# Optimization experiments

Hardware: AMD Instinct MI355X
Metric: run time of the kernel (lower is better)

## Reference

```python
import jax, jax.numpy as jnp
import numpy as np

NUM_HEADS = 16  # init kwarg num_attention_heads


def setup_inputs() -> dict:
    key = jax.random.key(0)
    k1, k2, k3, k4 = jax.random.split(key, 4)
    B, T, E = 2, 2048, 1024
    query = jax.random.normal(k1, (B, T, E), dtype=jnp.float32)
    key_t = jax.random.normal(k2, (B, T, E), dtype=jnp.float32)
    value = jax.random.normal(k3, (B, T, E), dtype=jnp.float32)
    # final output projection (nn.Linear(hidden, hidden, bias=False)); torch stores [out,in]
    W_out = jax.random.normal(k4, (E, E), dtype=jnp.float32) * 0.02
    return {"query": query, "key": key_t, "value": value, "W_out": W_out}


def reference(query, key, value, W_out):
    # NOTE: in the source, the per-head q_i/k_i/v_i linear projections are
    # overwritten by reshapes of the raw inputs, so the qs/ks/vs weights are
    # dead code. Every head computes identical output; mean over heads is a
    # no-op. We reproduce that exact math here.
    B, T, E = query.shape
    H = NUM_HEADS
    d = E // H  # head_dim; also d_k used in the 1/sqrt(d_k) scaling

    def split_heads(x):  # [B,T,E] -> [B,H,T,d]
        return x.reshape(B, T, H, d).transpose(0, 2, 1, 3)

    q = split_heads(query)
    k = split_heads(key)
    v = split_heads(value)

    scale = jnp.sqrt(jnp.asarray(d, dtype=jnp.float32))
    scores = jnp.einsum('bhtd,bhsd->bhts', q, k) / scale  # [B,H,T,T]
    attn = jax.nn.softmax(scores, axis=-1)
    head = jnp.einsum('bhts,bhsd->bhtd', attn, v)         # [B,H,T,d]
    head = head.transpose(0, 2, 1, 3).reshape(B, T, E)    # concat heads

    # mean over H identical head outputs == head; final linear (no bias)
    outputs = head @ W_out.T                              # [B,T,E]
    # mean over H identical attention maps == attn, returned as [B*H,T,T]
    attention = attn.reshape(B * H, T, T)
    return outputs, attention
```

## Files before the change

kernel.cpp:

```cpp
#include <hip/hip_runtime.h>
#include <hip/hip_fp16.h>

#define B_NUM  2
#define T_DIM  2048
#define E_DIM  1024
#define H_NUM  16
#define D_HEAD 64
#define BH_NUM (B_NUM * H_NUM)
#define NT     (T_DIM / 64)

using half8  = __attribute__((ext_vector_type(8))) _Float16;
using half4v = __attribute__((ext_vector_type(4))) _Float16;
using f32x4  = __attribute__((ext_vector_type(4))) float;

#define AS1 __attribute__((address_space(1)))
#define AS3 __attribute__((address_space(3)))

#define QSCALE 0.18033688011112042f

#define BAR_VM(N)                                                       \
    do {                                                                \
        asm volatile("s_waitcnt vmcnt(" #N ")" ::: "memory");           \
        __builtin_amdgcn_s_barrier();                                   \
        __builtin_amdgcn_sched_barrier(0);                              \
    } while (0)

__device__ __forceinline__ void bar_plain() {
    __builtin_amdgcn_s_barrier();
    __builtin_amdgcn_sched_barrier(0);
}

#define TP_BLOCKS  (NT * BH_NUM)
#define CAST_BLOCKS 1280
__global__ void prep_kernel(const float* __restrict__ kin,
                            const float* __restrict__ win,
                            const float* __restrict__ V,
                            _Float16* __restrict__ Kh,
                            _Float16* __restrict__ Wh,
                            _Float16* __restrict__ Vt,
                            int nk4, int ntot4) {
    __shared__ float tile[64][65];
    int t = threadIdx.x;

    if (blockIdx.x < TP_BLOCKS) {
        int s0 = (blockIdx.x & 31) * 64;
        int bh = blockIdx.x >> 5;
        int b = bh >> 4, h = bh & 15;

        int row = t >> 2;
        int c0  = (t & 3) * 16;
        const float* src = V + ((size_t)(b * T_DIM + s0 + row)) * E_DIM + h * D_HEAD + c0;
#pragma unroll
        for (int j = 0; j < 16; j += 4) {
            float4 v = *reinterpret_cast<const float4*>(src + j);
            tile[row][c0 + j + 0] = v.x;
            tile[row][c0 + j + 1] = v.y;
            tile[row][c0 + j + 2] = v.z;
            tile[row][c0 + j + 3] = v.w;
        }
        __syncthreads();

        int d  = t >> 2;
        int sc = (t & 3) * 16;
        half8 h0, h1;
#pragma unroll
        for (int j = 0; j < 8; ++j) {
            h0[j] = (_Float16)tile[sc + j][d];
            h1[j] = (_Float16)tile[sc + 8 + j][d];
        }
        _Float16* dst = Vt + ((size_t)(bh * D_HEAD + d)) * T_DIM + s0 + sc;
        *reinterpret_cast<half8*>(dst)     = h0;
        *reinterpret_cast<half8*>(dst + 8) = h1;
    } else {
        int stride = CAST_BLOCKS * 256;
        for (int i = (blockIdx.x - TP_BLOCKS) * 256 + t; i < ntot4; i += stride) {
            const float* src = (i < nk4) ? kin : win;
            _Float16* dst    = (i < nk4) ? Kh  : Wh;
            int j            = (i < nk4) ? i   : i - nk4;
            float4 v = reinterpret_cast<const float4*>(src)[j];
            half4v hh;
            hh[0] = (_Float16)v.x; hh[1] = (_Float16)v.y;
            hh[2] = (_Float16)v.z; hh[3] = (_Float16)v.w;
            reinterpret_cast<half4v*>(dst)[j] = hh;
        }
    }
}

__device__ __forceinline__ void stage_gl(const _Float16* __restrict__ g,
                                         size_t stride, _Float16* lds,
                                         int w, int lane) {
    int r0 = lane >> 3;
    int c  = (lane & 7) ^ r0;
#pragma unroll
    for (int j = 0; j < 2; ++j) {
        int r = (w + 4 * j) * 8 + r0;
        const _Float16* src = g + (size_t)r * stride + c * 8;
        _Float16* dst = lds + (w + 4 * j) * 512;
        __builtin_amdgcn_global_load_lds((const AS1 void*)src, (AS3 void*)dst,
                                         16, 0, 0);
    }
}

__device__ __forceinline__ half8 read_frag64(const _Float16* lds, int row, int chunk) {
    int csw = chunk ^ (row & 7);
    return *reinterpret_cast<const half8*>(lds + row * 64 + csw * 8);
}

__device__ __forceinline__ void load_qfrag(const float* qsrc, int lg, half8* qf) {
#pragma unroll
    for (int ks = 0; ks < 2; ++ks) {
        float4 a0 = *reinterpret_cast<const float4*>(qsrc + (lg + 4 * ks) * 8);
        float4 a1 = *reinterpret_cast<const float4*>(qsrc + (lg + 4 * ks) * 8 + 4);
        qf[ks][0] = (_Float16)(a0.x * QSCALE); qf[ks][1] = (_Float16)(a0.y * QSCALE);
        qf[ks][2] = (_Float16)(a0.z * QSCALE); qf[ks][3] = (_Float16)(a0.w * QSCALE);
        qf[ks][4] = (_Float16)(a1.x * QSCALE); qf[ks][5] = (_Float16)(a1.y * QSCALE);
        qf[ks][6] = (_Float16)(a1.z * QSCALE); qf[ks][7] = (_Float16)(a1.w * QSCALE);
    }
}

__global__ __launch_bounds__(256) void attn_kernel(
        const float* __restrict__ Q, const _Float16* __restrict__ Kh,
        const _Float16* __restrict__ Vt, float* __restrict__ attn_out,
        _Float16* __restrict__ head_h) {
    __shared__ __align__(16) _Float16 kbuf[2][64 * 64];
    __shared__ __align__(16) _Float16 vbuf[2][64 * 64];
    __shared__ __align__(16) _Float16 pbuf[4][16 * 64];

    int tid  = threadIdx.x;
    int wq   = tid >> 6;
    int lane = tid & 63;
    int l15  = lane & 15;
    int lg   = lane >> 4;

    int flat = blockIdx.x;
    int bh   = (flat & 7) * 4 + (flat >> 8);
    int qt   = (flat >> 3) & 31;
    int q0   = qt * 64;
    int b = bh >> 4, h = bh & 15;

    const float* qsrc = Q + ((size_t)(b * T_DIM + q0 + wq * 16 + l15)) * E_DIM + h * D_HEAD;
    half8 qfrag[2];
    load_qfrag(qsrc, lg, qfrag);

    const _Float16* kg = Kh + ((size_t)b * T_DIM) * E_DIM + h * D_HEAD;
    const _Float16* vg = Vt + (size_t)bh * D_HEAD * T_DIM;

#define P1TILE(KB)                                                             \
    {                                                                          \
        f32x4 acc[4];                                                          \
        _Pragma("unroll")                                                      \
        for (int ct = 0; ct < 4; ++ct) acc[ct] = (f32x4){0.f, 0.f, 0.f, 0.f};  \
        __builtin_amdgcn_s_setprio(1);                                         \
        _Pragma("unroll")                                                      \
        for (int ks = 0; ks < 2; ++ks)                                         \
            _Pragma("unroll")                                                  \
            for (int ct = 0; ct < 4; ++ct) {                                   \
                half8 kf = read_frag64((KB), ct * 16 + l15, lg + 4 * ks);      \
                acc[ct] = __builtin_amdgcn_mfma_f32_16x16x32_f16(              \
                    kf, qfrag[ks], acc[ct], 0, 0, 0);                          \
            }                                                                  \
        __builtin_amdgcn_s_setprio(0);                                         \
        _Pragma("unroll")                                                      \
        for (int ct = 0; ct < 4; ++ct)                                         \
            _Pragma("unroll")                                                  \
            for (int r = 0; r < 4; ++r)                                        \
                lsum += __builtin_amdgcn_exp2f(acc[ct][r]);                    \
    }

    int rot2 = (qt << 1) & 31;
#define IDX1(n) (((n) + rot2) & 31)
    float lsum = 0.0f;
    stage_gl(kg + (size_t)IDX1(0) * 64 * E_DIM, E_DIM, kbuf[0], wq, lane);
    stage_gl(kg + (size_t)IDX1(1) * 64 * E_DIM, E_DIM, kbuf[1], wq, lane);
    for (int tt = 0; tt < NT / 2; tt += 2) {
        {
            stage_gl(kg + (size_t)IDX1(2 * tt + 2) * 64 * E_DIM, E_DIM, vbuf[0], wq, lane);
            stage_gl(kg + (size_t)IDX1(2 * tt + 3) * 64 * E_DIM, E_DIM, vbuf[1], wq, lane);
            BAR_VM(4);
            P1TILE(kbuf[0]);
            P1TILE(kbuf[1]);
            bar_plain();
        }
        {
            if (tt + 2 < NT / 2) {
                stage_gl(kg + (size_t)IDX1(2 * tt + 4) * 64 * E_DIM, E_DIM, kbuf[0], wq, lane);
                stage_gl(kg + (size_t)IDX1(2 * tt + 5) * 64 * E_DIM, E_DIM, kbuf[1], wq, lane);
                BAR_VM(4);
            } else {
                BAR_VM(0);
            }
            P1TILE(vbuf[0]);
            P1TILE(vbuf[1]);
            bar_plain();
        }
    }
#undef IDX1

    lsum += __shfl_xor(lsum, 16);
    lsum += __shfl_xor(lsum, 32);
    float rl = 1.0f / lsum;

    f32x4 oacc[4];
#pragma unroll
    for (int cd = 0; cd < 4; ++cd) oacc[cd] = (f32x4){0.f, 0.f, 0.f, 0.f};

    float* ab = attn_out + (size_t)bh * T_DIM * T_DIM;
    _Float16* pw = pbuf[wq];
    int myq = q0 + wq * 16 + l15;

    int cur = 0;
    {
        int p0 = qt & 31;
        stage_gl(kg + (size_t)p0 * 64 * E_DIM, E_DIM, kbuf[0], wq, lane);
        stage_gl(vg + p0 * 64, T_DIM, vbuf[0], wq, lane);
    }
    for (int t = 0; t < NT; ++t) {
        int phys = (t + qt) & 31;
        if (t < NT - 1) {
            int pn = (t + 1 + qt) & 31;
            stage_gl(kg + (size_t)pn * 64 * E_DIM, E_DIM, kbuf[cur ^ 1], wq, lane);
            stage_gl(vg + pn * 64, T_DIM, vbuf[cur ^ 1], wq, lane);
        }
        if (t == 0)           BAR_VM(4);
        else if (t < NT - 1)  BAR_VM(8);
        else                  BAR_VM(4);
        const _Float16* kb = kbuf[cur];
        const _Float16* vb = vbuf[cur];

        f32x4 acc[4];
#pragma unroll
        for (int ct = 0; ct < 4; ++ct) acc[ct] = (f32x4){0.f, 0.f, 0.f, 0.f};
        __builtin_amdgcn_s_setprio(1);
#pragma unroll
        for (int ks = 0; ks < 2; ++ks)
#pragma unroll
            for (int ct = 0; ct < 4; ++ct) {
                half8 kf = read_frag64(kb, ct * 16 + l15, lg + 4 * ks);
                acc[ct] = __builtin_amdgcn_mfma_f32_16x16x32_f16(kf, qfrag[ks], acc[ct], 0, 0, 0);
            }
        __builtin_amdgcn_s_setprio(0);

        float* abrow = ab + (size_t)myq * T_DIM + phys * 64 + lg * 4;
#pragma unroll
        for (int ct = 0; ct < 4; ++ct) {
            f32x4 p;
            p[0] = __builtin_amdgcn_exp2f(acc[ct][0]) * rl;
            p[1] = __builtin_amdgcn_exp2f(acc[ct][1]) * rl;
            p[2] = __builtin_amdgcn_exp2f(acc[ct][2]) * rl;
            p[3] = __builtin_amdgcn_exp2f(acc[ct][3]) * rl;
            *reinterpret_cast<f32x4*>(abrow + ct * 16) = p;
            half4v ph;
            ph[0] = (_Float16)p[0]; ph[1] = (_Float16)p[1];
            ph[2] = (_Float16)p[2]; ph[3] = (_Float16)p[3];
            int cc = (ct * 4 + lg) ^ l15;
            *reinterpret_cast<half4v*>(pw + l15 * 64 + cc * 4) = ph;
        }

        __builtin_amdgcn_s_setprio(1);
#pragma unroll
        for (int ks = 0; ks < 2; ++ks) {
            int c0 = 2 * (lg + 4 * ks);
            half4v lo = *reinterpret_cast<const half4v*>(pw + l15 * 64 + ((c0)     ^ l15) * 4);
            half4v hi = *reinterpret_cast<const half4v*>(pw + l15 * 64 + ((c0 + 1) ^ l15) * 4);
            half8 pa;
            pa[0] = lo[0]; pa[1] = lo[1]; pa[2] = lo[2]; pa[3] = lo[3];
            pa[4] = hi[0]; pa[5] = hi[1]; pa[6] = hi[2]; pa[7] = hi[3];
#pragma unroll
            for (int cd = 0; cd < 4; ++cd) {
                half8 vf = read_frag64(vb, cd * 16 + l15, lg + 4 * ks);
                oacc[cd] = __builtin_amdgcn_mfma_f32_16x16x32_f16(pa, vf, oacc[cd], 0, 0, 0);
            }
        }
        __builtin_amdgcn_s_setprio(0);
        bar_plain();
        cur ^= 1;
    }

    _Float16* hw = head_h + ((size_t)(b * T_DIM + q0 + wq * 16)) * E_DIM + h * D_HEAD;
#pragma unroll
    for (int cd = 0; cd < 4; ++cd)
#pragma unroll
        for (int r = 0; r < 4; ++r) {
            int qm = lg * 4 + r;
            hw[(size_t)qm * E_DIM + cd * 16 + l15] = (_Float16)oacc[cd][r];
        }
#undef P1TILE
}

__global__ __launch_bounds__(256) void proj_kernel(
        const _Float16* __restrict__ A, const _Float16* __restrict__ Wh,
        float* __restrict__ out) {
    __shared__ __align__(16) _Float16 abuf[2][64 * 64];
    __shared__ __align__(16) _Float16 bbuf[2][64 * 64];

    int tid  = threadIdx.x;
    int wq   = tid >> 6;
    int lane = tid & 63;
    int l15  = lane & 15;
    int lg   = lane >> 4;

    int m0 = blockIdx.x * 64;
    int n0 = blockIdx.y * 64;

    f32x4 acc[4];
#pragma unroll
    for (int ct = 0; ct < 4; ++ct) acc[ct] = (f32x4){0.f, 0.f, 0.f, 0.f};

    int cur = 0;
    stage_gl(A  + (size_t)m0 * E_DIM, E_DIM, abuf[0], wq, lane);
    stage_gl(Wh + (size_t)n0 * E_DIM, E_DIM, bbuf[0], wq, lane);
    for (int t = 0; t < E_DIM / 64; ++t) {
        if (t + 1 < E_DIM / 64) {
            stage_gl(A  + (size_t)m0 * E_DIM + (t + 1) * 64, E_DIM, abuf[cur ^ 1], wq, lane);
            stage_gl(Wh + (size_t)n0 * E_DIM + (t + 1) * 64, E_DIM, bbuf[cur ^ 1], wq, lane);
            BAR_VM(4);
        } else {
            BAR_VM(0);
        }
#pragma unroll
        for (int ks = 0; ks < 2; ++ks) {
            half8 hf = read_frag64(abuf[cur], wq * 16 + l15, lg + 4 * ks);
#pragma unroll
            for (int ct = 0; ct < 4; ++ct) {
                half8 wf = read_frag64(bbuf[cur], ct * 16 + l15, lg + 4 * ks);
                acc[ct] = __builtin_amdgcn_mfma_f32_16x16x32_f16(wf, hf, acc[ct], 0, 0, 0);
            }
        }
        bar_plain();
        cur ^= 1;
    }

    float* orow = out + (size_t)(m0 + wq * 16 + l15) * E_DIM + n0 + lg * 4;
#pragma unroll
    for (int ct = 0; ct < 4; ++ct) {
        f32x4 o;
        o[0] = acc[ct][0]; o[1] = acc[ct][1]; o[2] = acc[ct][2]; o[3] = acc[ct][3];
        *reinterpret_cast<f32x4*>(orow + ct * 16) = o;
    }
}

extern "C" void kernel_launch(void* const* d_in, const int* in_sizes, int n_in,
                              void* d_out, int out_size, void* d_ws, size_t ws_size,
                              hipStream_t stream) {
    const float* q = (const float*)d_in[0];
    const float* k = (const float*)d_in[1];
    const float* v = (const float*)d_in[2];
    const float* w = (const float*)d_in[3];

    float* outs = (float*)d_out;
    float* attn = outs + (size_t)B_NUM * T_DIM * E_DIM;

    char* ws = (char*)d_ws;
    _Float16* Kh = (_Float16*)(ws);
    _Float16* Vt = (_Float16*)(ws + (size_t)(8  << 20));
    _Float16* Wh = (_Float16*)(ws + (size_t)(16 << 20));
    _Float16* Hh = (_Float16*)(ws + (size_t)(18 << 20));

    int nk4 = B_NUM * T_DIM * E_DIM / 4;
    int nw4 = E_DIM * E_DIM / 4;

    prep_kernel<<<TP_BLOCKS + CAST_BLOCKS, 256, 0, stream>>>(
        k, w, v, Kh, Wh, Vt, nk4, nk4 + nw4);
    attn_kernel<<<NT * BH_NUM, 256, 0, stream>>>(q, Kh, Vt, attn, Hh);
    proj_kernel<<<dim3((B_NUM * T_DIM) / 64, E_DIM / 64), 256, 0, stream>>>(Hh, Wh, outs);
}
```

Before: 183.5 us.

## Use five-slot ring buffer for softmax-denominator pass, reuse smem across phases

Replaces the separate K/V/P shared buffers with one 5-slot shared pool. The first pass, which computes row sums, now streams K tiles through a 5-deep ring with a prefetch distance of three and one barrier per tile, replacing the double-buffered pairs with two barriers per pair. The second pass reuses the same slots for K, V and P. The goal is to hide more global load latency in pass one and keep shared memory usage the same or lower. The trade-off is a selection chain to pick the ring slot and an extra barrier between the phases.

```diff
diff --git a/kernel.cpp b/kernel.cpp
--- a/kernel.cpp
+++ b/kernel.cpp
@@ -122,9 +122,8 @@
         const float* __restrict__ Q, const _Float16* __restrict__ Kh,
         const _Float16* __restrict__ Vt, float* __restrict__ attn_out,
         _Float16* __restrict__ head_h) {
-    __shared__ __align__(16) _Float16 kbuf[2][64 * 64];
-    __shared__ __align__(16) _Float16 vbuf[2][64 * 64];
-    __shared__ __align__(16) _Float16 pbuf[4][16 * 64];
+    __shared__ __align__(16) _Float16 smem[5 * 4096];
+#define SLOTP(s) (smem + (s) * 4096)
 
     int tid  = threadIdx.x;
     int wq   = tid >> 6;
@@ -167,34 +166,35 @@
                 lsum += __builtin_amdgcn_exp2f(acc[ct][r]);                    \
     }
 
-    int rot2 = (qt << 1) & 31;
-#define IDX1(n) (((n) + rot2) & 31)
+#define SLOTSEL(s) ((s) == 0 ? SLOTP(0) : (s) == 1 ? SLOTP(1) :                \
+                    (s) == 2 ? SLOTP(2) : (s) == 3 ? SLOTP(3) : SLOTP(4))
+
     float lsum = 0.0f;
-    stage_gl(kg + (size_t)IDX1(0) * 64 * E_DIM, E_DIM, kbuf[0], wq, lane);
-    stage_gl(kg + (size_t)IDX1(1) * 64 * E_DIM, E_DIM, kbuf[1], wq, lane);
-    for (int tt = 0; tt < NT / 2; tt += 2) {
-        {
-            stage_gl(kg + (size_t)IDX1(2 * tt + 2) * 64 * E_DIM, E_DIM, vbuf[0], wq, lane);
-            stage_gl(kg + (size_t)IDX1(2 * tt + 3) * 64 * E_DIM, E_DIM, vbuf[1], wq, lane);
-            BAR_VM(4);
-            P1TILE(kbuf[0]);
-            P1TILE(kbuf[1]);
-            bar_plain();
-        }
-        {
-            if (tt + 2 < NT / 2) {
-                stage_gl(kg + (size_t)IDX1(2 * tt + 4) * 64 * E_DIM, E_DIM, kbuf[0], wq, lane);
-                stage_gl(kg + (size_t)IDX1(2 * tt + 5) * 64 * E_DIM, E_DIM, kbuf[1], wq, lane);
-                BAR_VM(4);
-            } else {
-                BAR_VM(0);
-            }
-            P1TILE(vbuf[0]);
-            P1TILE(vbuf[1]);
-            bar_plain();
-        }
-    }
+    {
+#define IDX1(n) (((n) + qt) & 31)
+        stage_gl(kg + (size_t)IDX1(0) * 64 * E_DIM, E_DIM, SLOTP(0), wq, lane);
+        stage_gl(kg + (size_t)IDX1(1) * 64 * E_DIM, E_DIM, SLOTP(1), wq, lane);
+        stage_gl(kg + (size_t)IDX1(2) * 64 * E_DIM, E_DIM, SLOTP(2), wq, lane);
+        int ss = 3, sc = 0;
+        for (int t = 0; t <= NT - 4; ++t) {
+            _Float16* sp = SLOTSEL(ss);
+            stage_gl(kg + (size_t)IDX1(t + 3) * 64 * E_DIM, E_DIM, sp, wq, lane);
+            BAR_VM(6);
+            const _Float16* cp = SLOTSEL(sc);
+            P1TILE(cp);
+            ss = (ss == 4) ? 0 : ss + 1;
+            sc = (sc == 4) ? 0 : sc + 1;
+        }
+        BAR_VM(4);
+        { const _Float16* cp = SLOTSEL(sc); P1TILE(cp); }
+        sc = (sc == 4) ? 0 : sc + 1;
+        BAR_VM(2);
+        { const _Float16* cp = SLOTSEL(sc); P1TILE(cp); }
+        sc = (sc == 4) ? 0 : sc + 1;
+        BAR_VM(0);
+        { const _Float16* cp = SLOTSEL(sc); P1TILE(cp); }
 #undef IDX1
+    }
 
     lsum += __shfl_xor(lsum, 16);
     lsum += __shfl_xor(lsum, 32);
@@ -205,27 +205,31 @@
     for (int cd = 0; cd < 4; ++cd) oacc[cd] = (f32x4){0.f, 0.f, 0.f, 0.f};
 
     float* ab = attn_out + (size_t)bh * T_DIM * T_DIM;
-    _Float16* pw = pbuf[wq];
+    _Float16* pw = SLOTP(4) + wq * 1024;
     int myq = q0 + wq * 16 + l15;
+
+    bar_plain();
 
     int cur = 0;
     {
         int p0 = qt & 31;
-        stage_gl(kg + (size_t)p0 * 64 * E_DIM, E_DIM, kbuf[0], wq, lane);
-        stage_gl(vg + p0 * 64, T_DIM, vbuf[0], wq, lane);
+        stage_gl(kg + (size_t)p0 * 64 * E_DIM, E_DIM, SLOTP(0), wq, lane);
+        stage_gl(vg + p0 * 64, T_DIM, SLOTP(2), wq, lane);
     }
     for (int t = 0; t < NT; ++t) {
         int phys = (t + qt) & 31;
         if (t < NT - 1) {
             int pn = (t + 1 + qt) & 31;
-            stage_gl(kg + (size_t)pn * 64 * E_DIM, E_DIM, kbuf[cur ^ 1], wq, lane);
-            stage_gl(vg + pn * 64, T_DIM, vbuf[cur ^ 1], wq, lane);
+            _Float16* kn = cur ? SLOTP(0) : SLOTP(1);
+            _Float16* vn = cur ? SLOTP(2) : SLOTP(3);
+            stage_gl(kg + (size_t)pn * 64 * E_DIM, E_DIM, kn, wq, lane);
+            stage_gl(vg + pn * 64, T_DIM, vn, wq, lane);
         }
         if (t == 0)           BAR_VM(4);
         else if (t < NT - 1)  BAR_VM(8);
         else                  BAR_VM(4);
-        const _Float16* kb = kbuf[cur];
-        const _Float16* vb = vbuf[cur];
+        const _Float16* kb = cur ? SLOTP(1) : SLOTP(0);
+        const _Float16* vb = cur ? SLOTP(3) : SLOTP(2);
 
         f32x4 acc[4];
 #pragma unroll
@@ -285,6 +289,8 @@
             hw[(size_t)qm * E_DIM + cd * 16 + l15] = (_Float16)oacc[cd][r];
         }
 #undef P1TILE
+#undef SLOTSEL
+#undef SLOTP
 }
 
 __global__ __launch_bounds__(256) void proj_kernel(
```

After: 187.2 us. 2.0% more time.
